# Kernel tuning notes

Measured on AMD Instinct MI355X. Metric: run time of the kernel, lower is better.

Reference implementation:

```python
import jax, jax.numpy as jnp
import numpy as np

MARGIN = 0.1


def setup_inputs() -> dict:
    key = jax.random.key(0)
    k1, k2 = jax.random.split(key)
    N, M, C = 16384, 16384, 512
    return {
        "features_view1": jax.random.normal(k1, (N, C), dtype=jnp.float32),
        "features_view2": jax.random.normal(k2, (M, C), dtype=jnp.float32),
    }


def reference(features_view1, features_view2):
    # torch.cdist(p=2) via the matmul identity ||a-b||^2 = |a|^2 + |b|^2 - 2 a.b
    sq1 = jnp.sum(features_view1 * features_view1, axis=1, keepdims=True)  # [N,1]
    sq2 = jnp.sum(features_view2 * features_view2, axis=1)                 # [M]
    inner = features_view1 @ features_view2.T                              # [N,M]
    dist2 = jnp.maximum(sq1 + sq2[None, :] - 2.0 * inner, 0.0)
    nn_dist = jnp.sqrt(jnp.min(dist2, axis=1))                             # [N]
    return jnp.mean(jax.nn.relu(nn_dist - MARGIN))
```

## Files before the change

kernel.cpp:

```cpp
#include <hip/hip_runtime.h>
#include <stdint.h>

#define N_ROWS 16384
#define M_ROWS 16384
#define KDIM   512
#define BM 128
#define BNT 64
#define BKP 128
#define NCHUNK 8
#define CHUNK_ROWS (M_ROWS / NCHUNK)
#define BT_PER_CHUNK (CHUNK_ROWS / BNT)

typedef int intx4 __attribute__((ext_vector_type(4)));
typedef int intx8 __attribute__((ext_vector_type(8)));
typedef float floatx4 __attribute__((ext_vector_type(4)));

#define UNIT_SCALE 0x7F7F7F7F

__device__ __forceinline__ void async_ld16(const uint8_t* g, uint8_t* l) {
  __builtin_amdgcn_global_load_lds(
      (const __attribute__((address_space(1))) void*)g,
      (__attribute__((address_space(3))) void*)l, 16, 0, 0);
}

__global__ void conv_kernel(const float* __restrict__ A, const float* __restrict__ B,
                            uint8_t* __restrict__ Ah8, uint8_t* __restrict__ Bh8,
                            float* __restrict__ sq1, float* __restrict__ sq2) {
  const int lane = threadIdx.x & 63;
  const int wv = threadIdx.x >> 6;
  int row = blockIdx.x * 4 + wv;
  const float* src;
  uint8_t* dst;
  float* sq;
  if (row < N_ROWS) {
    src = A + (size_t)row * KDIM;
    dst = Ah8 + (size_t)row * KDIM;
    sq = sq1 + row;
  } else {
    int r = row - N_ROWS;
    src = B + (size_t)r * KDIM;
    dst = Bh8 + (size_t)r * KDIM;
    sq = sq2 + r;
  }
  const float4* s4 = (const float4*)src;
  float4 v0 = s4[lane * 2];
  float4 v1 = s4[lane * 2 + 1];
  uint32_t w0 = 0, w1 = 0;
  w0 = __builtin_amdgcn_cvt_pk_fp8_f32(v0.x, v0.y, w0, 0);
  w0 = __builtin_amdgcn_cvt_pk_fp8_f32(v0.z, v0.w, w0, 1);
  w1 = __builtin_amdgcn_cvt_pk_fp8_f32(v1.x, v1.y, w1, 0);
  w1 = __builtin_amdgcn_cvt_pk_fp8_f32(v1.z, v1.w, w1, 1);
  uint2 pk = {w0, w1};
  ((uint2*)dst)[lane] = pk;
  float s = v0.x * v0.x + v0.y * v0.y + v0.z * v0.z + v0.w * v0.w
          + v1.x * v1.x + v1.y * v1.y + v1.z * v1.z + v1.w * v1.w;
  #pragma unroll
  for (int off = 32; off; off >>= 1) s += __shfl_down(s, off, 64);
  if (lane == 0) *sq = s;
}

__global__ void __launch_bounds__(128, 2)
gemm_min_kernel(const uint8_t* __restrict__ Ah8, const uint8_t* __restrict__ Bh8,
                const float* __restrict__ sq2, float* __restrict__ ws_min) {
  __shared__ __align__(16) uint8_t lsB[2][BNT * BKP];

  const int tid = threadIdx.x;
  const int lane = tid & 63;
  const int wv = tid >> 6;
  const int fr = lane & 15;
  const int kg = lane >> 4;
  const int frs = fr & 7;

  const int bid = blockIdx.x;
  const int chunk = bid & 7;
  const int rowBase = (bid >> 3) * BM;
  const int colBase0 = chunk * CHUNK_ROWS;

  const int cis = lane >> 3;
  const int kofs_st = (((lane & 7) ^ cis) << 4);

  intx8 areg[4][4];
  {
    const uint8_t* abase = Ah8 + (size_t)(rowBase + wv * 64 + fr) * KDIM + kg * 32;
    #pragma unroll
    for (int i = 0; i < 4; i++)
      #pragma unroll
      for (int p = 0; p < 4; p++) {
        const uint8_t* ap = abase + (size_t)i * 16 * KDIM + p * BKP;
        intx4 lo = *(const intx4*)ap;
        intx4 hi = *(const intx4*)(ap + 16);
        areg[i][p] = __builtin_shufflevector(lo, hi, 0, 1, 2, 3, 4, 5, 6, 7);
      }
  }

  float runmin[4][4];
  #pragma unroll
  for (int i = 0; i < 4; i++)
    #pragma unroll
    for (int r4 = 0; r4 < 4; r4++) runmin[i][r4] = 3.0e38f;

  #define STAGE_B(buf, cb, kbase_)                                            \
    {                                                                         \
      _Pragma("unroll")                                                       \
      for (int c = 0; c < 4; ++c) {                                           \
        const int slot = wv * 4 + c;                                          \
        async_ld16(Bh8 + (size_t)((cb) + slot * 8 + cis) * KDIM +             \
                       (kbase_) + kofs_st,                                    \
                   (buf) + (slot << 10));                                     \
      }                                                                       \
    }

  STAGE_B(lsB[0], colBase0, 0)
  __syncthreads();

  for (int bt = 0; bt < BT_PER_CHUNK; ++bt) {
    const int colBase = colBase0 + bt * BNT;
    floatx4 acc[4][4];
    #pragma unroll
    for (int i = 0; i < 4; i++)
      #pragma unroll
      for (int j = 0; j < 4; j++) acc[i][j] = (floatx4){0.f, 0.f, 0.f, 0.f};

    #pragma unroll
    for (int p = 0; p < 4; ++p) {
      const uint8_t* cur = lsB[p & 1];
      if (p < 3) {
        STAGE_B(lsB[(p + 1) & 1], colBase, (p + 1) * BKP)
      } else if (bt + 1 < BT_PER_CHUNK) {
        STAGE_B(lsB[0], colBase + BNT, 0)
      }
      #pragma unroll
      for (int j = 0; j < 4; j++) {
        const uint8_t* bp = cur + (j * 16 + fr) * BKP;
        intx4 lo = *(const intx4*)(bp + ((((kg << 1)) ^ frs) << 4));
        intx4 hi = *(const intx4*)(bp + ((((kg << 1) | 1) ^ frs) << 4));
        intx8 bv = __builtin_shufflevector(lo, hi, 0, 1, 2, 3, 4, 5, 6, 7);
        #pragma unroll
        for (int i = 0; i < 4; i++)
          acc[i][j] = __builtin_amdgcn_mfma_scale_f32_16x16x128_f8f6f4(
              areg[i][p], bv, acc[i][j], 0, 0,
              0, UNIT_SCALE, 0, UNIT_SCALE);
      }
      __syncthreads();
    }

    #pragma unroll
    for (int j = 0; j < 4; j++) {
      const float s2 = sq2[colBase + j * 16 + fr];
      #pragma unroll
      for (int i = 0; i < 4; i++)
        #pragma unroll
        for (int r4 = 0; r4 < 4; r4++) {
          const float cand = fmaf(-2.f, acc[i][j][r4], s2);
          runmin[i][r4] = fminf(runmin[i][r4], cand);
        }
    }
  }

  #pragma unroll
  for (int i = 0; i < 4; i++)
    #pragma unroll
    for (int r4 = 0; r4 < 4; r4++) {
      float v = runmin[i][r4];
      v = fminf(v, __shfl_xor(v, 1, 64));
      v = fminf(v, __shfl_xor(v, 2, 64));
      v = fminf(v, __shfl_xor(v, 4, 64));
      v = fminf(v, __shfl_xor(v, 8, 64));
      runmin[i][r4] = v;
    }

  if (fr == 0) {
    #pragma unroll
    for (int i = 0; i < 4; i++)
      #pragma unroll
      for (int r4 = 0; r4 < 4; r4++) {
        const int lrow = wv * 64 + i * 16 + kg * 4 + r4;
        ws_min[(size_t)chunk * N_ROWS + rowBase + lrow] = runmin[i][r4];
      }
  }
}

__global__ void partial_kernel(const float* __restrict__ ws_min,
                               const float* __restrict__ sq1,
                               float* __restrict__ part) {
  const int r = blockIdx.x * 256 + threadIdx.x;
  float m = ws_min[r];
  #pragma unroll
  for (int c = 1; c < NCHUNK; c++) m = fminf(m, ws_min[(size_t)c * N_ROWS + r]);
  float d2 = sq1[r] + m;
  d2 = d2 > 0.f ? d2 : 0.f;
  float v = sqrtf(d2) - 0.1f;
  float s = v > 0.f ? v : 0.f;
  #pragma unroll
  for (int off = 32; off; off >>= 1) s += __shfl_down(s, off, 64);
  __shared__ float ps[4];
  if ((threadIdx.x & 63) == 0) ps[threadIdx.x >> 6] = s;
  __syncthreads();
  if (threadIdx.x == 0) part[blockIdx.x] = ps[0] + ps[1] + ps[2] + ps[3];
}

__global__ void final_kernel(const float* __restrict__ part, float* __restrict__ out) {
  float s = part[threadIdx.x];
  #pragma unroll
  for (int off = 32; off; off >>= 1) s += __shfl_down(s, off, 64);
  if (threadIdx.x == 0) out[0] = s / (float)N_ROWS;
}

extern "C" void kernel_launch(void* const* d_in, const int* in_sizes, int n_in,
                              void* d_out, int out_size, void* d_ws, size_t ws_size,
                              hipStream_t stream) {
  const float* A = (const float*)d_in[0];
  const float* B = (const float*)d_in[1];
  char* ws = (char*)d_ws;
  const size_t fp8Bytes = (size_t)N_ROWS * KDIM;
  uint8_t* Ah8 = (uint8_t*)ws;
  uint8_t* Bh8 = (uint8_t*)(ws + fp8Bytes);
  float* sq1 = (float*)(ws + 2 * fp8Bytes);
  float* sq2 = sq1 + N_ROWS;
  float* ws_min = sq2 + M_ROWS;
  float* part = ws_min + (size_t)NCHUNK * N_ROWS;

  conv_kernel<<<dim3((N_ROWS + M_ROWS) / 4), dim3(256), 0, stream>>>(A, B, Ah8, Bh8, sq1, sq2);
  gemm_min_kernel<<<dim3((N_ROWS / BM) * NCHUNK), dim3(128), 0, stream>>>(Ah8, Bh8, sq2, ws_min);
  partial_kernel<<<dim3(64), dim3(256), 0, stream>>>(ws_min, sq1, part);
  final_kernel<<<dim3(1), dim3(64), 0, stream>>>(part, (float*)d_out);
}
```

Before: 208.8 us.

## Deepen B staging to four LDS buffers with explicit vmcnt waits

```diff
diff --git a/kernel.cpp b/kernel.cpp
--- a/kernel.cpp
+++ b/kernel.cpp
@@ -62,7 +62,8 @@
 __global__ void __launch_bounds__(128, 2)
 gemm_min_kernel(const uint8_t* __restrict__ Ah8, const uint8_t* __restrict__ Bh8,
                 const float* __restrict__ sq2, float* __restrict__ ws_min) {
-  __shared__ __align__(16) uint8_t lsB[2][BNT * BKP];
+  __shared__ __align__(16) uint8_t lsB[4][BNT * BKP];
+  __shared__ __align__(16) float sq2_lds[CHUNK_ROWS];
 
   const int tid = threadIdx.x;
   const int lane = tid & 63;
@@ -110,8 +111,17 @@
       }                                                                       \
     }
 
+  {
+    const uint8_t* s2src = (const uint8_t*)(sq2 + colBase0);
+    #pragma unroll
+    for (int c = 0; c < 4; ++c) {
+      const int off = ((wv * 4 + c) << 10);
+      async_ld16(s2src + off + lane * 16, ((uint8_t*)sq2_lds) + off);
+    }
+  }
   STAGE_B(lsB[0], colBase0, 0)
-  __syncthreads();
+  STAGE_B(lsB[1], colBase0, BKP)
+  STAGE_B(lsB[2], colBase0, 2 * BKP)
 
   for (int bt = 0; bt < BT_PER_CHUNK; ++bt) {
     const int colBase = colBase0 + bt * BNT;
@@ -123,12 +133,27 @@
 
     #pragma unroll
     for (int p = 0; p < 4; ++p) {
-      const uint8_t* cur = lsB[p & 1];
-      if (p < 3) {
-        STAGE_B(lsB[(p + 1) & 1], colBase, (p + 1) * BKP)
+      if (p >= 2 && bt == BT_PER_CHUNK - 1) {
+        if (p == 2) {
+          asm volatile("s_waitcnt vmcnt(4)" ::: "memory");
+        } else {
+          asm volatile("s_waitcnt vmcnt(0)" ::: "memory");
+        }
+      } else {
+        asm volatile("s_waitcnt vmcnt(8)" ::: "memory");
+      }
+      __builtin_amdgcn_s_barrier();
+      asm volatile("" ::: "memory");
+      __builtin_amdgcn_sched_barrier(0);
+
+      if (p == 0) {
+        STAGE_B(lsB[3], colBase, 3 * BKP)
       } else if (bt + 1 < BT_PER_CHUNK) {
-        STAGE_B(lsB[0], colBase + BNT, 0)
-      }
+        STAGE_B(lsB[(p + 3) & 3], colBase + BNT, (p - 1) * BKP)
+      }
+
+      const uint8_t* cur = lsB[p];
+      __builtin_amdgcn_s_setprio(1);
       #pragma unroll
       for (int j = 0; j < 4; j++) {
         const uint8_t* bp = cur + (j * 16 + fr) * BKP;
@@ -141,12 +166,12 @@
               areg[i][p], bv, acc[i][j], 0, 0,
               0, UNIT_SCALE, 0, UNIT_SCALE);
       }
-      __syncthreads();
+      __builtin_amdgcn_s_setprio(0);
     }
 
     #pragma unroll
     for (int j = 0; j < 4; j++) {
-      const float s2 = sq2[colBase + j * 16 + fr];
+      const float s2 = sq2_lds[bt * BNT + j * 16 + fr];
       #pragma unroll
       for (int i = 0; i < 4; i++)
         #pragma unroll
```

Measured after the change: 207.9 us. No clear change (-0.4%).
